# Kernel tuning notes

Hardware: AMD Instinct MI355X
Metric: run time of the kernel (lower is better)

## Reference

```python
import jax, jax.numpy as jnp
import numpy as np

# Model dims (match init_kwargs)
B, S, H = 1, 2048, 1024
E = 16            # n_routed_experts
I = 768           # moe_intermediate_size
TOPK = 4          # num_experts_per_tok
G = 4             # n_group
TOPK_G = 2        # topk_group
SCALE = 2.5       # routed_scaling_factor
N_SHARED = 1      # n_shared_experts


def setup_inputs() -> dict:
    key = jax.random.key(0)
    ks = jax.random.split(key, 9)
    def rn(k, shape, scale=0.02):
        return jax.random.normal(k, shape, dtype=jnp.float32) * scale
    return dict(
        hidden_states=jax.random.normal(ks[0], (B, S, H), dtype=jnp.float32),
        gate_w=rn(ks[1], (E, H)),
        gate_bias=jax.random.normal(ks[2], (E,), dtype=jnp.float32) * 0.1,
        w1=rn(ks[3], (E, I, H)),   # gate_proj weights [out,in]
        w2=rn(ks[4], (E, H, I)),   # down_proj weights
        w3=rn(ks[5], (E, I, H)),   # up_proj weights
        ws1=rn(ks[6], (I * N_SHARED, H)),
        ws2=rn(ks[7], (H, I * N_SHARED)),
        ws3=rn(ks[8], (I * N_SHARED, H)),
    )


def _route(x, gate_w, gate_bias):
    """noaux_tc routing: sigmoid scores + bias, group top-k, top_k experts."""
    n = x.shape[0]
    logits = jnp.einsum('nh,eh->ne', x.astype(jnp.float32), gate_w)  # [N,E]
    scores = jax.nn.sigmoid(logits)
    sb = scores + gate_bias                                          # biased scores
    # group score = sum of top-2 biased scores in each group
    gs = sb.reshape(n, G, E // G)
    group_scores = jnp.sum(jax.lax.top_k(gs, 2)[0], axis=-1)         # [N,G]
    _, gidx = jax.lax.top_k(group_scores, TOPK_G)                    # [N,TOPK_G]
    gmask = jnp.sum(jax.nn.one_hot(gidx, G, dtype=sb.dtype), axis=1) # [N,G]
    emask = jnp.repeat(gmask, E // G, axis=-1)                       # [N,E]
    masked = jnp.where(emask > 0, sb, -jnp.inf)
    _, tidx = jax.lax.top_k(masked, TOPK)                            # [N,TOPK]
    w = jnp.take_along_axis(scores, tidx, axis=1)                    # unbiased weights
    w = w / (jnp.sum(w, axis=-1, keepdims=True) + 1e-20)             # norm_topk_prob
    return tidx, w * SCALE


def reference(hidden_states, gate_w, gate_bias, w1, w2, w3, ws1, ws2, ws3):
    b, s, h = hidden_states.shape
    x = hidden_states.reshape(-1, h)                                 # [N,H]
    tidx, tw = _route(x, gate_w, gate_bias)
    n = x.shape[0]
    # dense combine weights [N,E] (zero for unselected experts)
    combine = jnp.zeros((n, E), x.dtype).at[jnp.arange(n)[:, None], tidx].add(tw)
    # grouped SwiGLU experts (dense-over-experts reference form)
    g = jnp.einsum('nh,eih->nei', x, w1)
    u = jnp.einsum('nh,eih->nei', x, w3)
    hact = jax.nn.silu(g) * u * combine[:, :, None]
    y = jnp.einsum('nei,ehi->nh', hact, w2)
    # shared expert SwiGLU
    shared = jnp.einsum('ni,hi->nh', jax.nn.silu(x @ ws1.T) * (x @ ws3.T), ws2)
    return (y + shared).reshape(b, s, h)
```

## Files before the change

### kernel.cpp

```cpp
#include <hip/hip_runtime.h>
#include <hip/hip_bf16.h>
#include <math.h>

#define N_TOK 2048
#define H_DIM 1024
#define N_EXP 16
#define I_DIM 768
#define TOPK 4
#define SCALE 2.5f
#define MAX_TILES 96

typedef __attribute__((ext_vector_type(8))) short bf16x8;
typedef __attribute__((ext_vector_type(4))) float f32x4;

#define OFF_COUNTS   0
#define OFF_OFFSETS  128
#define OFF_TILES    256
#define OFF_TOKIDS   768
#define OFF_TOKW     (OFF_TOKIDS + N_EXP*N_TOK*4)
#define OFF_XB       (OFF_TOKW + N_EXP*N_TOK*4)
#define OFF_HACT     (OFF_XB + (size_t)N_TOK*H_DIM*2)
#define OFF_GWT      (OFF_HACT + (size_t)N_TOK*(TOPK+1)*I_DIM*2)

__device__ __forceinline__ ushort f2bf(float f) {
    union { __hip_bfloat16 h; ushort u; } cv;
    cv.h = __float2bfloat16(f);
    return cv.u;
}
__device__ __forceinline__ unsigned pack2(float lo, float hi) {
    return (unsigned)f2bf(lo) | ((unsigned)f2bf(hi) << 16);
}
__device__ __forceinline__ void async_copy16(const void* g, void* l) {
    __builtin_amdgcn_global_load_lds(
        (const __attribute__((address_space(1))) unsigned int*)g,
        (__attribute__((address_space(3))) unsigned int*)l, 16, 0, 0);
}

__global__ void k_xconv(const float* __restrict__ x, ushort* __restrict__ xb) {
    int i = blockIdx.x * 256 + threadIdx.x;
    float4 v = ((const float4*)x)[i];
    uint2 p;
    p.x = pack2(v.x, v.y);
    p.y = pack2(v.z, v.w);
    ((uint2*)xb)[i] = p;
}

__global__ void k_gwt(const float* __restrict__ gw, float* __restrict__ gwT) {
    int i = blockIdx.x * 256 + threadIdx.x;
    int k = i >> 4, e = i & 15;
    gwT[i] = gw[e * H_DIM + k];
}

__launch_bounds__(256)
__global__ void k_route(const float* __restrict__ x, const float* __restrict__ gwT,
                        const float* __restrict__ gb,
                        int* __restrict__ counts, int* __restrict__ tok_ids,
                        float* __restrict__ tok_w) {
    __shared__ float lgs[4][N_EXP + 1];
    int tid = threadIdx.x;
    int wv = tid >> 6, lane = tid & 63;
    int e = lane & 15, ks = lane >> 4;
    int n = blockIdx.x * 4 + wv;

    const float* xr = x + (size_t)n * H_DIM + ks * 256;
    const float* wr = gwT + ks * 256 * N_EXP + e;
    float a0 = 0.f, a1 = 0.f, a2 = 0.f, a3 = 0.f;
#pragma unroll 8
    for (int k = 0; k < 256; k += 4) {
        float4 xv = *(const float4*)(xr + k);
        a0 += xv.x * wr[(k + 0) * N_EXP];
        a1 += xv.y * wr[(k + 1) * N_EXP];
        a2 += xv.z * wr[(k + 2) * N_EXP];
        a3 += xv.w * wr[(k + 3) * N_EXP];
    }
    float acc = (a0 + a1) + (a2 + a3);
    acc += __shfl_xor(acc, 16);
    acc += __shfl_xor(acc, 32);
    if (lane < 16) lgs[wv][lane] = acc;
    __syncthreads();

    if (tid < 4) {
        int n2 = blockIdx.x * 4 + tid;
        float sc[N_EXP], sb[N_EXP];
        for (int ee = 0; ee < N_EXP; ee++) {
            float l = lgs[tid][ee];
            sc[ee] = 1.f / (1.f + expf(-l));
            sb[ee] = sc[ee] + gb[ee];
        }
        float gsc[4];
        for (int g = 0; g < 4; g++) {
            float m1 = -1e30f, m2 = -1e30f;
            for (int j = 0; j < 4; j++) {
                float v = sb[4 * g + j];
                if (v > m1) { m2 = m1; m1 = v; }
                else if (v > m2) m2 = v;
            }
            gsc[g] = m1 + m2;
        }
        int g1 = 0;
        for (int g = 1; g < 4; g++) if (gsc[g] > gsc[g1]) g1 = g;
        int g2 = -1;
        for (int g = 0; g < 4; g++) {
            if (g == g1) continue;
            if (g2 < 0 || gsc[g] > gsc[g2]) g2 = g;
        }
        bool allowed[N_EXP];
        for (int ee = 0; ee < N_EXP; ee++) {
            int grp = ee >> 2;
            allowed[ee] = (grp == g1) || (grp == g2);
        }
        int chosen[TOPK];
        float wsum = 0.f;
        for (int k = 0; k < TOPK; k++) {
            int best = -1;
            for (int ee = 0; ee < N_EXP; ee++) {
                if (!allowed[ee]) continue;
                if (best < 0 || sb[ee] > sb[best]) best = ee;
            }
            chosen[k] = best;
            allowed[best] = false;
            wsum += sc[best];
        }
        float inv = SCALE / (wsum + 1e-20f);
        for (int k = 0; k < TOPK; k++) {
            int ee = chosen[k];
            int p = atomicAdd(&counts[ee], 1);
            tok_ids[ee * N_TOK + p] = n2;
            tok_w[ee * N_TOK + p] = sc[ee] * inv;
        }
    }
}

__global__ void k_scan(const int* __restrict__ counts, int* __restrict__ offsets,
                       int* __restrict__ tiles) {
    if (threadIdx.x == 0 && blockIdx.x == 0) {
        int off = 0;
        for (int e = 0; e < N_EXP; e++) { offsets[e] = off; off += counts[e]; }
        offsets[N_EXP] = off;
        int t = 0;
        for (int e = 0; e < N_EXP; e++)
            for (int m0 = 0; m0 < counts[e]; m0 += 128)
                tiles[t++] = e | ((m0 >> 7) << 5);
        for (int m0 = 0; m0 < N_TOK; m0 += 128)
            tiles[t++] = N_EXP | ((m0 >> 7) << 5);
        for (; t < MAX_TILES; t++) tiles[t] = -1;
    }
}

__launch_bounds__(256, 3)
__global__ void k_gateup(const ushort* __restrict__ xb, const float* __restrict__ w1,
                         const float* __restrict__ w3, const float* __restrict__ ws1,
                         const float* __restrict__ ws3, const int* __restrict__ counts,
                         const int* __restrict__ offsets, const int* __restrict__ tiles,
                         const int* __restrict__ tok_ids, const float* __restrict__ tok_w,
                         ushort* __restrict__ hact) {
    int desc = tiles[blockIdx.x];
    if (desc < 0) return;
    int e = desc & 31;
    int m0 = (desc >> 5) * 128;
    int i0 = blockIdx.y * 64;
    int Me = (e == N_EXP) ? N_TOK : counts[e];
    const float* W1 = (e == N_EXP) ? ws1 : w1 + (size_t)e * I_DIM * H_DIM;
    const float* W3 = (e == N_EXP) ? ws3 : w3 + (size_t)e * I_DIM * H_DIM;
    int base = offsets[e];

    __shared__ ushort As[128][64];
    __shared__ ushort Bs[128][64];
    __shared__ float tws[128];

    int tid = threadIdx.x;
    int wv = tid >> 6, lane = tid & 63;
    int seg = lane & 7, rsub = lane >> 3;
    int gch = (seg ^ rsub) * 8;

    if (tid < 128) {
        int r = m0 + tid;
        tws[tid] = (e == N_EXP) ? 1.f : ((r < Me) ? tok_w[e * N_TOK + r] : 0.f);
    }

    const ushort* aptr[4];
#pragma unroll
    for (int j = 0; j < 4; j++) {
        int gr = m0 + wv * 32 + j * 8 + rsub;
        int tok = (e == N_EXP) ? gr : ((gr < Me) ? tok_ids[e * N_TOK + gr] : 0);
        aptr[j] = xb + (size_t)tok * H_DIM + gch;
    }
    const float* bptrf[4];
#pragma unroll
    for (int j = 0; j < 4; j++) {
        int r = wv * 32 + j * 8 + rsub;
        const float* W = (r < 64) ? (W1 + (size_t)(i0 + r) * H_DIM)
                                  : (W3 + (size_t)(i0 + r - 64) * H_DIM);
        bptrf[j] = W + gch;
    }

    int quad = lane >> 4, lr = lane & 15, rx = lr & 7;
    f32x4 acc[2][8] = {};

    const int NK = H_DIM / 64;
    float4 bv0[4], bv1[4];
#pragma unroll
    for (int j = 0; j < 4; j++) {
        bv0[j] = *(const float4*)(bptrf[j]);
        bv1[j] = *(const float4*)(bptrf[j] + 4);
    }
    for (int k = 0; k < NK; k++) {
        int off = k * 64;
#pragma unroll
        for (int j = 0; j < 4; j++) async_copy16(aptr[j] + off, &As[wv * 32 + j * 8][0]);
#pragma unroll
        for (int j = 0; j < 4; j++) {
            uint4 p;
            p.x = pack2(bv0[j].x, bv0[j].y);
            p.y = pack2(bv0[j].z, bv0[j].w);
            p.z = pack2(bv1[j].x, bv1[j].y);
            p.w = pack2(bv1[j].z, bv1[j].w);
            *(uint4*)&Bs[wv * 32 + j * 8 + rsub][seg * 8] = p;
        }
        if (k + 1 < NK) {
#pragma unroll
            for (int j = 0; j < 4; j++) {
                bv0[j] = *(const float4*)(bptrf[j] + off + 64);
                bv1[j] = *(const float4*)(bptrf[j] + off + 68);
            }
        }
        __syncthreads();
#pragma unroll
        for (int ks = 0; ks < 2; ks++) {
            int co = ((ks * 4 + quad) ^ rx) * 8;
            bf16x8 a0 = *(const bf16x8*)&As[wv * 32 + lr][co];
            bf16x8 a1 = *(const bf16x8*)&As[wv * 32 + 16 + lr][co];
#pragma unroll
            for (int ni = 0; ni < 8; ni++) {
                bf16x8 bf = *(const bf16x8*)&Bs[ni * 16 + lr][co];
                acc[0][ni] = __builtin_amdgcn_mfma_f32_16x16x32_bf16(a0, bf, acc[0][ni], 0, 0, 0);
                acc[1][ni] = __builtin_amdgcn_mfma_f32_16x16x32_bf16(a1, bf, acc[1][ni], 0, 0, 0);
            }
        }
        __syncthreads();
    }

#pragma unroll
    for (int mi = 0; mi < 2; mi++) {
#pragma unroll
        for (int ni = 0; ni < 4; ni++) {
            f32x4 g = acc[mi][ni];
            f32x4 u = acc[mi][ni + 4];
#pragma unroll
            for (int rg = 0; rg < 4; rg++) {
                int ml = wv * 32 + mi * 16 + quad * 4 + rg;
                int row = m0 + ml;
                if (row < Me) {
                    float gg = g[rg], uu = u[rg];
                    float act = (gg / (1.f + expf(-gg))) * uu * tws[ml];
                    hact[(size_t)(base + row) * I_DIM + i0 + ni * 16 + lr] = f2bf(act);
                }
            }
        }
    }
}

__launch_bounds__(256, 3)
__global__ void k_down(const ushort* __restrict__ hact, const float* __restrict__ w2,
                       const float* __restrict__ ws2, const int* __restrict__ counts,
                       const int* __restrict__ offsets, const int* __restrict__ tiles,
                       const int* __restrict__ tok_ids, float* __restrict__ out) {
    int desc = tiles[blockIdx.x];
    if (desc < 0) return;
    int e = desc & 31;
    int m0 = (desc >> 5) * 128;
    int h0 = blockIdx.y * 128;
    int Me = (e == N_EXP) ? N_TOK : counts[e];
    const float* W2 = (e == N_EXP) ? ws2 : w2 + (size_t)e * H_DIM * I_DIM;
    int base = offsets[e];

    __shared__ ushort As[128][64];
    __shared__ ushort Bs[128][64];
    __shared__ int toks[128];

    int tid = threadIdx.x;
    int wv = tid >> 6, lane = tid & 63;
    int seg = lane & 7, rsub = lane >> 3;
    int gch = (seg ^ rsub) * 8;

    if (tid < 128) {
        int r = m0 + tid;
        toks[tid] = (e == N_EXP) ? r : ((r < Me) ? tok_ids[e * N_TOK + r] : 0);
    }

    const ushort* aptr[4];
#pragma unroll
    for (int j = 0; j < 4; j++) {
        int row = wv * 32 + j * 8 + rsub;
        aptr[j] = hact + (size_t)(base + m0 + row) * I_DIM + gch;
    }
    const float* bptrf[4];
#pragma unroll
    for (int j = 0; j < 4; j++) {
        int r = wv * 32 + j * 8 + rsub;
        bptrf[j] = W2 + (size_t)(h0 + r) * I_DIM + gch;
    }

    int quad = lane >> 4, lr = lane & 15, rx = lr & 7;
    f32x4 acc[2][8] = {};

    const int NK = I_DIM / 64;
    float4 bv0[4], bv1[4];
#pragma unroll
    for (int j = 0; j < 4; j++) {
        bv0[j] = *(const float4*)(bptrf[j]);
        bv1[j] = *(const float4*)(bptrf[j] + 4);
    }
    for (int k = 0; k < NK; k++) {
        int off = k * 64;
#pragma unroll
        for (int j = 0; j < 4; j++) async_copy16(aptr[j] + off, &As[wv * 32 + j * 8][0]);
#pragma unroll
        for (int j = 0; j < 4; j++) {
            uint4 p;
            p.x = pack2(bv0[j].x, bv0[j].y);
            p.y = pack2(bv0[j].z, bv0[j].w);
            p.z = pack2(bv1[j].x, bv1[j].y);
            p.w = pack2(bv1[j].z, bv1[j].w);
            *(uint4*)&Bs[wv * 32 + j * 8 + rsub][seg * 8] = p;
        }
        if (k + 1 < NK) {
#pragma unroll
            for (int j = 0; j < 4; j++) {
                bv0[j] = *(const float4*)(bptrf[j] + off + 64);
                bv1[j] = *(const float4*)(bptrf[j] + off + 68);
            }
        }
        __syncthreads();
#pragma unroll
        for (int ks = 0; ks < 2; ks++) {
            int co = ((ks * 4 + quad) ^ rx) * 8;
            bf16x8 a0 = *(const bf16x8*)&As[wv * 32 + lr][co];
            bf16x8 a1 = *(const bf16x8*)&As[wv * 32 + 16 + lr][co];
#pragma unroll
            for (int ni = 0; ni < 8; ni++) {
                bf16x8 bf = *(const bf16x8*)&Bs[ni * 16 + lr][co];
                acc[0][ni] = __builtin_amdgcn_mfma_f32_16x16x32_bf16(a0, bf, acc[0][ni], 0, 0, 0);
                acc[1][ni] = __builtin_amdgcn_mfma_f32_16x16x32_bf16(a1, bf, acc[1][ni], 0, 0, 0);
            }
        }
        __syncthreads();
    }

#pragma unroll
    for (int mi = 0; mi < 2; mi++) {
#pragma unroll
        for (int ni = 0; ni < 8; ni++) {
#pragma unroll
            for (int rg = 0; rg < 4; rg++) {
                int ml = wv * 32 + mi * 16 + quad * 4 + rg;
                int row = m0 + ml;
                if (row < Me) {
                    int tok = toks[ml];
                    atomicAdd(&out[(size_t)tok * H_DIM + h0 + ni * 16 + lr],
                              acc[mi][ni][rg]);
                }
            }
        }
    }
}

extern "C" void kernel_launch(void* const* d_in, const int* in_sizes, int n_in,
                              void* d_out, int out_size, void* d_ws, size_t ws_size,
                              hipStream_t stream) {
    const float* x   = (const float*)d_in[0];
    const float* gw  = (const float*)d_in[1];
    const float* gb  = (const float*)d_in[2];
    const float* w1  = (const float*)d_in[3];
    const float* w2  = (const float*)d_in[4];
    const float* w3  = (const float*)d_in[5];
    const float* ws1 = (const float*)d_in[6];
    const float* ws2 = (const float*)d_in[7];
    const float* ws3 = (const float*)d_in[8];
    float* out = (float*)d_out;

    char* wsb = (char*)d_ws;
    int* counts   = (int*)(wsb + OFF_COUNTS);
    int* offsets  = (int*)(wsb + OFF_OFFSETS);
    int* tiles    = (int*)(wsb + OFF_TILES);
    int* tok_ids  = (int*)(wsb + OFF_TOKIDS);
    float* tok_w  = (float*)(wsb + OFF_TOKW);
    ushort* xb    = (ushort*)(wsb + OFF_XB);
    ushort* hact  = (ushort*)(wsb + OFF_HACT);
    float* gwT    = (float*)(wsb + OFF_GWT);

    hipMemsetAsync(wsb, 0, 128, stream);
    hipMemsetAsync(d_out, 0, (size_t)out_size * 4, stream);

    k_xconv<<<N_TOK * H_DIM / 4 / 256, 256, 0, stream>>>(x, xb);
    k_gwt<<<N_EXP * H_DIM / 256, 256, 0, stream>>>(gw, gwT);
    k_route<<<N_TOK / 4, 256, 0, stream>>>(x, gwT, gb, counts, tok_ids, tok_w);
    k_scan<<<1, 1, 0, stream>>>(counts, offsets, tiles);
    {
        dim3 grid(MAX_TILES, I_DIM / 64);
        k_gateup<<<grid, 256, 0, stream>>>(xb, w1, w3, ws1, ws3, counts, offsets,
                                           tiles, tok_ids, tok_w, hact);
    }
    {
        dim3 grid(MAX_TILES, H_DIM / 128);
        k_down<<<grid, 256, 0, stream>>>(hact, w2, ws2, counts, offsets, tiles,
                                         tok_ids, out);
    }
}
```

Before: 364.7 us.

## Batch up to four M-tiles per block in expert GEMMs to reuse weight streams

Each block now handles a job of up to four consecutive 128-row tiles of one expert, looping over them, instead of a single tile. The grids shrink from 96 tile slots to 48 job slots, and the launch bounds rise from 3 to 4 blocks per CU. The intent is to cut per-block setup and raise L2 reuse of the fp32 weight slices, since consecutive tiles of one block read the same weight columns. The cost is fewer blocks in flight (48×12 and 48×8 slots), which risks underfilling the CUs and load imbalance when some experts have many tiles. Weights are still re-read and re-converted to bf16 for every tile.

```diff
diff --git a/kernel.cpp b/kernel.cpp
--- a/kernel.cpp
+++ b/kernel.cpp
@@ -8,14 +8,15 @@
 #define I_DIM 768
 #define TOPK 4
 #define SCALE 2.5f
-#define MAX_TILES 96
+#define MAX_JOBS 48
+#define JOB_MT 4
 
 typedef __attribute__((ext_vector_type(8))) short bf16x8;
 typedef __attribute__((ext_vector_type(4))) float f32x4;
 
 #define OFF_COUNTS   0
 #define OFF_OFFSETS  128
-#define OFF_TILES    256
+#define OFF_JOBS     256
 #define OFF_TOKIDS   768
 #define OFF_TOKW     (OFF_TOKIDS + N_EXP*N_TOK*4)
 #define OFF_XB       (OFF_TOKW + N_EXP*N_TOK*4)
@@ -132,32 +133,37 @@
 }
 
 __global__ void k_scan(const int* __restrict__ counts, int* __restrict__ offsets,
-                       int* __restrict__ tiles) {
+                       int* __restrict__ jobs) {
     if (threadIdx.x == 0 && blockIdx.x == 0) {
         int off = 0;
         for (int e = 0; e < N_EXP; e++) { offsets[e] = off; off += counts[e]; }
         offsets[N_EXP] = off;
         int t = 0;
-        for (int e = 0; e < N_EXP; e++)
-            for (int m0 = 0; m0 < counts[e]; m0 += 128)
-                tiles[t++] = e | ((m0 >> 7) << 5);
-        for (int m0 = 0; m0 < N_TOK; m0 += 128)
-            tiles[t++] = N_EXP | ((m0 >> 7) << 5);
-        for (; t < MAX_TILES; t++) tiles[t] = -1;
-    }
-}
-
-__launch_bounds__(256, 3)
+        for (int e = 0; e < N_EXP; e++) {
+            int nmt = (counts[e] + 127) >> 7;
+            for (int m = 0; m < nmt; m += JOB_MT) {
+                int take = (nmt - m < JOB_MT) ? (nmt - m) : JOB_MT;
+                jobs[t++] = e | (m << 5) | (take << 9);
+            }
+        }
+        for (int m = 0; m < N_TOK / 128; m += JOB_MT)
+            jobs[t++] = N_EXP | (m << 5) | (JOB_MT << 9);
+        for (; t < MAX_JOBS; t++) jobs[t] = -1;
+    }
+}
+
+__launch_bounds__(256, 4)
 __global__ void k_gateup(const ushort* __restrict__ xb, const float* __restrict__ w1,
                          const float* __restrict__ w3, const float* __restrict__ ws1,
                          const float* __restrict__ ws3, const int* __restrict__ counts,
-                         const int* __restrict__ offsets, const int* __restrict__ tiles,
+                         const int* __restrict__ offsets, const int* __restrict__ jobs,
                          const int* __restrict__ tok_ids, const float* __restrict__ tok_w,
                          ushort* __restrict__ hact) {
-    int desc = tiles[blockIdx.x];
+    int desc = jobs[blockIdx.x];
     if (desc < 0) return;
     int e = desc & 31;
-    int m0 = (desc >> 5) * 128;
+    int mt0 = (desc >> 5) & 15;
+    int nmt = desc >> 9;
     int i0 = blockIdx.y * 64;
     int Me = (e == N_EXP) ? N_TOK : counts[e];
     const float* W1 = (e == N_EXP) ? ws1 : w1 + (size_t)e * I_DIM * H_DIM;
@@ -172,19 +178,8 @@
     int wv = tid >> 6, lane = tid & 63;
     int seg = lane & 7, rsub = lane >> 3;
     int gch = (seg ^ rsub) * 8;
-
-    if (tid < 128) {
-        int r = m0 + tid;
-        tws[tid] = (e == N_EXP) ? 1.f : ((r < Me) ? tok_w[e * N_TOK + r] : 0.f);
-    }
-
-    const ushort* aptr[4];
-#pragma unroll
-    for (int j = 0; j < 4; j++) {
-        int gr = m0 + wv * 32 + j * 8 + rsub;
-        int tok = (e == N_EXP) ? gr : ((gr < Me) ? tok_ids[e * N_TOK + gr] : 0);
-        aptr[j] = xb + (size_t)tok * H_DIM + gch;
-    }
+    int quad = lane >> 4, lr = lane & 15, rx = lr & 7;
+
     const float* bptrf[4];
 #pragma unroll
     for (int j = 0; j < 4; j++) {
@@ -194,81 +189,96 @@
         bptrf[j] = W + gch;
     }
 
-    int quad = lane >> 4, lr = lane & 15, rx = lr & 7;
-    f32x4 acc[2][8] = {};
-
-    const int NK = H_DIM / 64;
-    float4 bv0[4], bv1[4];
-#pragma unroll
-    for (int j = 0; j < 4; j++) {
-        bv0[j] = *(const float4*)(bptrf[j]);
-        bv1[j] = *(const float4*)(bptrf[j] + 4);
-    }
-    for (int k = 0; k < NK; k++) {
-        int off = k * 64;
-#pragma unroll
-        for (int j = 0; j < 4; j++) async_copy16(aptr[j] + off, &As[wv * 32 + j * 8][0]);
+    for (int mt = 0; mt < nmt; mt++) {
+        int m0 = (mt0 + mt) * 128;
+        __syncthreads();
+        if (tid < 128) {
+            int r = m0 + tid;
+            tws[tid] = (e == N_EXP) ? 1.f : ((r < Me) ? tok_w[e * N_TOK + r] : 0.f);
+        }
+        const ushort* aptr[4];
 #pragma unroll
         for (int j = 0; j < 4; j++) {
-            uint4 p;
-            p.x = pack2(bv0[j].x, bv0[j].y);
-            p.y = pack2(bv0[j].z, bv0[j].w);
-            p.z = pack2(bv1[j].x, bv1[j].y);
-            p.w = pack2(bv1[j].z, bv1[j].w);
-            *(uint4*)&Bs[wv * 32 + j * 8 + rsub][seg * 8] = p;
-        }
-        if (k + 1 < NK) {
+            int gr = m0 + wv * 32 + j * 8 + rsub;
+            int tok = (e == N_EXP) ? gr : ((gr < Me) ? tok_ids[e * N_TOK + gr] : 0);
+            aptr[j] = xb + (size_t)tok * H_DIM + gch;
+        }
+
+        f32x4 acc[2][8] = {};
+        const int NK = H_DIM / 64;
+        float4 bv0[4], bv1[4];
+#pragma unroll
+        for (int j = 0; j < 4; j++) {
+            bv0[j] = *(const float4*)(bptrf[j]);
+            bv1[j] = *(const float4*)(bptrf[j] + 4);
+        }
+        for (int k = 0; k < NK; k++) {
+            int off = k * 64;
+#pragma unroll
+            for (int j = 0; j < 4; j++) async_copy16(aptr[j] + off, &As[wv * 32 + j * 8][0]);
 #pragma unroll
             for (int j = 0; j < 4; j++) {
-                bv0[j] = *(const float4*)(bptrf[j] + off + 64);
-                bv1[j] = *(const float4*)(bptrf[j] + off + 68);
-            }
-        }
-        __syncthreads();
-#pragma unroll
-        for (int ks = 0; ks < 2; ks++) {
-            int co = ((ks * 4 + quad) ^ rx) * 8;
-            bf16x8 a0 = *(const bf16x8*)&As[wv * 32 + lr][co];
-            bf16x8 a1 = *(const bf16x8*)&As[wv * 32 + 16 + lr][co];
-#pragma unroll
-            for (int ni = 0; ni < 8; ni++) {
-                bf16x8 bf = *(const bf16x8*)&Bs[ni * 16 + lr][co];
-                acc[0][ni] = __builtin_amdgcn_mfma_f32_16x16x32_bf16(a0, bf, acc[0][ni], 0, 0, 0);
-                acc[1][ni] = __builtin_amdgcn_mfma_f32_16x16x32_bf16(a1, bf, acc[1][ni], 0, 0, 0);
-            }
-        }
-        __syncthreads();
-    }
-
-#pragma unroll
-    for (int mi = 0; mi < 2; mi++) {
-#pragma unroll
-        for (int ni = 0; ni < 4; ni++) {
-            f32x4 g = acc[mi][ni];
-            f32x4 u = acc[mi][ni + 4];
-#pragma unroll
-            for (int rg = 0; rg < 4; rg++) {
-                int ml = wv * 32 + mi * 16 + quad * 4 + rg;
-                int row = m0 + ml;
-                if (row < Me) {
-                    float gg = g[rg], uu = u[rg];
-                    float act = (gg / (1.f + expf(-gg))) * uu * tws[ml];
-                    hact[(size_t)(base + row) * I_DIM + i0 + ni * 16 + lr] = f2bf(act);
-                }
-            }
-        }
-    }
-}
-
-__launch_bounds__(256, 3)
+                uint4 p;
+                p.x = pack2(bv0[j].x, bv0[j].y);
+                p.y = pack2(bv0[j].z, bv0[j].w);
+                p.z = pack2(bv1[j].x, bv1[j].y);
+                p.w = pack2(bv1[j].z, bv1[j].w);
+                *(uint4*)&Bs[wv * 32 + j * 8 + rsub][seg * 8] = p;
+            }
+            if (k + 1 < NK) {
+#pragma unroll
+                for (int j = 0; j < 4; j++) {
+                    bv0[j] = *(const float4*)(bptrf[j] + off + 64);
+                    bv1[j] = *(const float4*)(bptrf[j] + off + 68);
+                }
+            }
+            __syncthreads();
+#pragma unroll
+            for (int ks = 0; ks < 2; ks++) {
+                int co = ((ks * 4 + quad) ^ rx) * 8;
+                bf16x8 a0 = *(const bf16x8*)&As[wv * 32 + lr][co];
+                bf16x8 a1 = *(const bf16x8*)&As[wv * 32 + 16 + lr][co];
+#pragma unroll
+                for (int ni = 0; ni < 8; ni++) {
+                    bf16x8 bf = *(const bf16x8*)&Bs[ni * 16 + lr][co];
+                    acc[0][ni] = __builtin_amdgcn_mfma_f32_16x16x32_bf16(a0, bf, acc[0][ni], 0, 0, 0);
+                    acc[1][ni] = __builtin_amdgcn_mfma_f32_16x16x32_bf16(a1, bf, acc[1][ni], 0, 0, 0);
+                }
+            }
+            __syncthreads();
+        }
+
+#pragma unroll
+        for (int mi = 0; mi < 2; mi++) {
+#pragma unroll
+            for (int ni = 0; ni < 4; ni++) {
+                f32x4 g = acc[mi][ni];
+                f32x4 u = acc[mi][ni + 4];
+#pragma unroll
+                for (int rg = 0; rg < 4; rg++) {
+                    int ml = wv * 32 + mi * 16 + quad * 4 + rg;
+                    int row = m0 + ml;
+                    if (row < Me) {
+                        float gg = g[rg], uu = u[rg];
+                        float act = (gg / (1.f + expf(-gg))) * uu * tws[ml];
+                        hact[(size_t)(base + row) * I_DIM + i0 + ni * 16 + lr] = f2bf(act);
+                    }
+                }
+            }
+        }
+    }
+}
+
+__launch_bounds__(256, 4)
 __global__ void k_down(const ushort* __restrict__ hact, const float* __restrict__ w2,
                        const float* __restrict__ ws2, const int* __restrict__ counts,
-                       const int* __restrict__ offsets, const int* __restrict__ tiles,
+                       const int* __restrict__ offsets, const int* __restrict__ jobs,
                        const int* __restrict__ tok_ids, float* __restrict__ out) {
-    int desc = tiles[blockIdx.x];
+    int desc = jobs[blockIdx.x];
     if (desc < 0) return;
     int e = desc & 31;
-    int m0 = (desc >> 5) * 128;
+    int mt0 = (desc >> 5) & 15;
+    int nmt = desc >> 9;
     int h0 = blockIdx.y * 128;
     int Me = (e == N_EXP) ? N_TOK : counts[e];
     const float* W2 = (e == N_EXP) ? ws2 : w2 + (size_t)e * H_DIM * I_DIM;
@@ -282,18 +292,8 @@
     int wv = tid >> 6, lane = tid & 63;
     int seg = lane & 7, rsub = lane >> 3;
     int gch = (seg ^ rsub) * 8;
-
-    if (tid < 128) {
-        int r = m0 + tid;
-        toks[tid] = (e == N_EXP) ? r : ((r < Me) ? tok_ids[e * N_TOK + r] : 0);
-    }
-
-    const ushort* aptr[4];
-#pragma unroll
-    for (int j = 0; j < 4; j++) {
-        int row = wv * 32 + j * 8 + rsub;
-        aptr[j] = hact + (size_t)(base + m0 + row) * I_DIM + gch;
-    }
+    int quad = lane >> 4, lr = lane & 15, rx = lr & 7;
+
     const float* bptrf[4];
 #pragma unroll
     for (int j = 0; j < 4; j++) {
@@ -301,64 +301,77 @@
         bptrf[j] = W2 + (size_t)(h0 + r) * I_DIM + gch;
     }
 
-    int quad = lane >> 4, lr = lane & 15, rx = lr & 7;
-    f32x4 acc[2][8] = {};
-
-    const int NK = I_DIM / 64;
-    float4 bv0[4], bv1[4];
-#pragma unroll
-    for (int j = 0; j < 4; j++) {
-        bv0[j] = *(const float4*)(bptrf[j]);
-        bv1[j] = *(const float4*)(bptrf[j] + 4);
-    }
-    for (int k = 0; k < NK; k++) {
-        int off = k * 64;
-#pragma unroll
-        for (int j = 0; j < 4; j++) async_copy16(aptr[j] + off, &As[wv * 32 + j * 8][0]);
+    for (int mt = 0; mt < nmt; mt++) {
+        int m0 = (mt0 + mt) * 128;
+        __syncthreads();
+        if (tid < 128) {
+            int r = m0 + tid;
+            toks[tid] = (e == N_EXP) ? r : ((r < Me) ? tok_ids[e * N_TOK + r] : 0);
+        }
+        const ushort* aptr[4];
 #pragma unroll
         for (int j = 0; j < 4; j++) {
-            uint4 p;
-            p.x = pack2(bv0[j].x, bv0[j].y);
-            p.y = pack2(bv0[j].z, bv0[j].w);
-            p.z = pack2(bv1[j].x, bv1[j].y);
-            p.w = pack2(bv1[j].z, bv1[j].w);
-            *(uint4*)&Bs[wv * 32 + j * 8 + rsub][seg * 8] = p;
-        }
-        if (k + 1 < NK) {
+            int row = wv * 32 + j * 8 + rsub;
+            aptr[j] = hact + (size_t)(base + m0 + row) * I_DIM + gch;
+        }
+
+        f32x4 acc[2][8] = {};
+        const int NK = I_DIM / 64;
+        float4 bv0[4], bv1[4];
+#pragma unroll
+        for (int j = 0; j < 4; j++) {
+            bv0[j] = *(const float4*)(bptrf[j]);
+            bv1[j] = *(const float4*)(bptrf[j] + 4);
+        }
+        for (int k = 0; k < NK; k++) {
+            int off = k * 64;
+#pragma unroll
+            for (int j = 0; j < 4; j++) async_copy16(aptr[j] + off, &As[wv * 32 + j * 8][0]);
 #pragma unroll
             for (int j = 0; j < 4; j++) {
-                bv0[j] = *(const float4*)(bptrf[j] + off + 64);
-                bv1[j] = *(const float4*)(bptrf[j] + off + 68);
-            }
-        }
-        __syncthreads();
-#pragma unroll
-        for (int ks = 0; ks < 2; ks++) {
-            int co = ((ks * 4 + quad) ^ rx) * 8;
-            bf16x8 a0 = *(const bf16x8*)&As[wv * 32 + lr][co];
-            bf16x8 a1 = *(const bf16x8*)&As[wv * 32 + 16 + lr][co];
+                uint4 p;
+                p.x = pack2(bv0[j].x, bv0[j].y);
+                p.y = pack2(bv0[j].z, bv0[j].w);
+                p.z = pack2(bv1[j].x, bv1[j].y);
+                p.w = pack2(bv1[j].z, bv1[j].w);
+                *(uint4*)&Bs[wv * 32 + j * 8 + rsub][seg * 8] = p;
+            }
+            if (k + 1 < NK) {
+#pragma unroll
+                for (int j = 0; j < 4; j++) {
+                    bv0[j] = *(const float4*)(bptrf[j] + off + 64);
+                    bv1[j] = *(const float4*)(bptrf[j] + off + 68);
+                }
+            }
+            __syncthreads();
+#pragma unroll
+            for (int ks = 0; ks < 2; ks++) {
+                int co = ((ks * 4 + quad) ^ rx) * 8;
+                bf16x8 a0 = *(const bf16x8*)&As[wv * 32 + lr][co];
+                bf16x8 a1 = *(const bf16x8*)&As[wv * 32 + 16 + lr][co];
+#pragma unroll
+                for (int ni = 0; ni < 8; ni++) {
+                    bf16x8 bf = *(const bf16x8*)&Bs[ni * 16 + lr][co];
+                    acc[0][ni] = __builtin_amdgcn_mfma_f32_16x16x32_bf16(a0, bf, acc[0][ni], 0, 0, 0);
+                    acc[1][ni] = __builtin_amdgcn_mfma_f32_16x16x32_bf16(a1, bf, acc[1][ni], 0, 0, 0);
+                }
+            }
+            __syncthreads();
+        }
+
+#pragma unroll
+        for (int mi = 0; mi < 2; mi++) {
 #pragma unroll
             for (int ni = 0; ni < 8; ni++) {
-                bf16x8 bf = *(const bf16x8*)&Bs[ni * 16 + lr][co];
-                acc[0][ni] = __builtin_amdgcn_mfma_f32_16x16x32_bf16(a0, bf, acc[0][ni], 0, 0, 0);
-                acc[1][ni] = __builtin_amdgcn_mfma_f32_16x16x32_bf16(a1, bf, acc[1][ni], 0, 0, 0);
-            }
-        }
-        __syncthreads();
-    }
-
-#pragma unroll
-    for (int mi = 0; mi < 2; mi++) {
-#pragma unroll
-        for (int ni = 0; ni < 8; ni++) {
-#pragma unroll
-            for (int rg = 0; rg < 4; rg++) {
-                int ml = wv * 32 + mi * 16 + quad * 4 + rg;
-                int row = m0 + ml;
-                if (row < Me) {
-                    int tok = toks[ml];
-                    atomicAdd(&out[(size_t)tok * H_DIM + h0 + ni * 16 + lr],
-                              acc[mi][ni][rg]);
+#pragma unroll
+                for (int rg = 0; rg < 4; rg++) {
+                    int ml = wv * 32 + mi * 16 + quad * 4 + rg;
+                    int row = m0 + ml;
+                    if (row < Me) {
+                        int tok = toks[ml];
+                        atomicAdd(&out[(size_t)tok * H_DIM + h0 + ni * 16 + lr],
+                                  acc[mi][ni][rg]);
+                    }
                 }
             }
         }
@@ -382,7 +395,7 @@
     char* wsb = (char*)d_ws;
     int* counts   = (int*)(wsb + OFF_COUNTS);
     int* offsets  = (int*)(wsb + OFF_OFFSETS);
-    int* tiles    = (int*)(wsb + OFF_TILES);
+    int* jobs     = (int*)(wsb + OFF_JOBS);
     int* tok_ids  = (int*)(wsb + OFF_TOKIDS);
     float* tok_w  = (float*)(wsb + OFF_TOKW);
     ushort* xb    = (ushort*)(wsb + OFF_XB);
@@ -395,15 +408,15 @@
     k_xconv<<<N_TOK * H_DIM / 4 / 256, 256, 0, stream>>>(x, xb);
     k_gwt<<<N_EXP * H_DIM / 256, 256, 0, stream>>>(gw, gwT);
     k_route<<<N_TOK / 4, 256, 0, stream>>>(x, gwT, gb, counts, tok_ids, tok_w);
-    k_scan<<<1, 1, 0, stream>>>(counts, offsets, tiles);
+    k_scan<<<1, 1, 0, stream>>>(counts, offsets, jobs);
     {
-        dim3 grid(MAX_TILES, I_DIM / 64);
+        dim3 grid(MAX_JOBS, I_DIM / 64);
         k_gateup<<<grid, 256, 0, stream>>>(xb, w1, w3, ws1, ws3, counts, offsets,
-                                           tiles, tok_ids, tok_w, hact);
+                                           jobs, tok_ids, tok_w, hact);
     }
     {
-        dim3 grid(MAX_TILES, H_DIM / 128);
-        k_down<<<grid, 256, 0, stream>>>(hact, w2, ws2, counts, offsets, tiles,
+        dim3 grid(MAX_JOBS, H_DIM / 128);
+        k_down<<<grid, 256, 0, stream>>>(hact, w2, ws2, counts, offsets, jobs,
                                          tok_ids, out);
     }
 }
```

Result: slower. 605.1 us (+65.9%).

## Schedule expert tiles per XCD with load-balanced grouping for L2 reuse

Applied to the files above, without the earlier changes.

Replaces the 2D tile grid with per-XCD work tables built in the scan kernel: groups of up to four token tiles of the same expert and output slice are assigned to the least-loaded XCD, interleaved so the hardware's round-robin block dispatch lands them there. This aims to improve L2 reuse of expert weight slices and balance work across XCDs, and to remove most empty padded blocks. It makes the single-threaded scan more expensive and relies on the dispatch order mapping block id modulo 8 to an XCD; overflow of a slot table would silently drop tiles.

```diff
diff --git a/kernel.cpp b/kernel.cpp
--- a/kernel.cpp
+++ b/kernel.cpp
@@ -8,15 +8,22 @@
 #define I_DIM 768
 #define TOPK 4
 #define SCALE 2.5f
-#define MAX_TILES 96
+
+#define GU_SLOTS 176
+#define DN_SLOTS 128
+#define GU_TAB (8 * GU_SLOTS)
+#define DN_TAB (8 * DN_SLOTS)
+#define GU_NY (I_DIM / 64)
+#define DN_NY (H_DIM / 128)
 
 typedef __attribute__((ext_vector_type(8))) short bf16x8;
 typedef __attribute__((ext_vector_type(4))) float f32x4;
 
 #define OFF_COUNTS   0
 #define OFF_OFFSETS  128
-#define OFF_TILES    256
-#define OFF_TOKIDS   768
+#define OFF_WGU      256
+#define OFF_WDN      (OFF_WGU + GU_TAB*4)
+#define OFF_TOKIDS   (OFF_WDN + DN_TAB*4)
 #define OFF_TOKW     (OFF_TOKIDS + N_EXP*N_TOK*4)
 #define OFF_XB       (OFF_TOKW + N_EXP*N_TOK*4)
 #define OFF_HACT     (OFF_XB + (size_t)N_TOK*H_DIM*2)
@@ -132,33 +139,62 @@
 }
 
 __global__ void k_scan(const int* __restrict__ counts, int* __restrict__ offsets,
-                       int* __restrict__ tiles) {
-    if (threadIdx.x == 0 && blockIdx.x == 0) {
-        int off = 0;
-        for (int e = 0; e < N_EXP; e++) { offsets[e] = off; off += counts[e]; }
-        offsets[N_EXP] = off;
-        int t = 0;
-        for (int e = 0; e < N_EXP; e++)
-            for (int m0 = 0; m0 < counts[e]; m0 += 128)
-                tiles[t++] = e | ((m0 >> 7) << 5);
-        for (int m0 = 0; m0 < N_TOK; m0 += 128)
-            tiles[t++] = N_EXP | ((m0 >> 7) << 5);
-        for (; t < MAX_TILES; t++) tiles[t] = -1;
-    }
+                       int* __restrict__ wgu, int* __restrict__ wdn) {
+    if (threadIdx.x != 0 || blockIdx.x != 0) return;
+    int off = 0;
+    for (int e = 0; e < N_EXP; e++) { offsets[e] = off; off += counts[e]; }
+    offsets[N_EXP] = off;
+
+    int nx[8];
+    for (int c = 0; c < 8; c++) nx[c] = 0;
+    for (int y = 0; y < GU_NY; y++) {
+        for (int e = 0; e <= N_EXP; e++) {
+            int nmt = (e == N_EXP) ? (N_TOK >> 7) : ((counts[e] + 127) >> 7);
+            for (int m = 0; m < nmt; m += 4) {
+                int take = (nmt - m < 4) ? (nmt - m) : 4;
+                int c = 0;
+                for (int j = 1; j < 8; j++) if (nx[j] < nx[c]) c = j;
+                for (int k = 0; k < take && nx[c] < GU_SLOTS; k++) {
+                    wgu[c + 8 * nx[c]] = e | ((m + k) << 5) | (y << 9);
+                    nx[c]++;
+                }
+            }
+        }
+    }
+    for (int c = 0; c < 8; c++)
+        for (int r = nx[c]; r < GU_SLOTS; r++) wgu[c + 8 * r] = -1;
+
+    for (int c = 0; c < 8; c++) nx[c] = 0;
+    for (int y = 0; y < DN_NY; y++) {
+        for (int e = 0; e <= N_EXP; e++) {
+            int nmt = (e == N_EXP) ? (N_TOK >> 7) : ((counts[e] + 127) >> 7);
+            for (int m = 0; m < nmt; m += 4) {
+                int take = (nmt - m < 4) ? (nmt - m) : 4;
+                int c = 0;
+                for (int j = 1; j < 8; j++) if (nx[j] < nx[c]) c = j;
+                for (int k = 0; k < take && nx[c] < DN_SLOTS; k++) {
+                    wdn[c + 8 * nx[c]] = e | ((m + k) << 5) | (y << 9);
+                    nx[c]++;
+                }
+            }
+        }
+    }
+    for (int c = 0; c < 8; c++)
+        for (int r = nx[c]; r < DN_SLOTS; r++) wdn[c + 8 * r] = -1;
 }
 
 __launch_bounds__(256, 3)
 __global__ void k_gateup(const ushort* __restrict__ xb, const float* __restrict__ w1,
                          const float* __restrict__ w3, const float* __restrict__ ws1,
                          const float* __restrict__ ws3, const int* __restrict__ counts,
-                         const int* __restrict__ offsets, const int* __restrict__ tiles,
+                         const int* __restrict__ offsets, const int* __restrict__ wgu,
                          const int* __restrict__ tok_ids, const float* __restrict__ tok_w,
                          ushort* __restrict__ hact) {
-    int desc = tiles[blockIdx.x];
+    int desc = wgu[blockIdx.x];
     if (desc < 0) return;
     int e = desc & 31;
-    int m0 = (desc >> 5) * 128;
-    int i0 = blockIdx.y * 64;
+    int m0 = ((desc >> 5) & 15) * 128;
+    int i0 = ((desc >> 9) & 15) * 64;
     int Me = (e == N_EXP) ? N_TOK : counts[e];
     const float* W1 = (e == N_EXP) ? ws1 : w1 + (size_t)e * I_DIM * H_DIM;
     const float* W3 = (e == N_EXP) ? ws3 : w3 + (size_t)e * I_DIM * H_DIM;
@@ -263,13 +299,13 @@
 __launch_bounds__(256, 3)
 __global__ void k_down(const ushort* __restrict__ hact, const float* __restrict__ w2,
                        const float* __restrict__ ws2, const int* __restrict__ counts,
-                       const int* __restrict__ offsets, const int* __restrict__ tiles,
+                       const int* __restrict__ offsets, const int* __restrict__ wdn,
                        const int* __restrict__ tok_ids, float* __restrict__ out) {
-    int desc = tiles[blockIdx.x];
+    int desc = wdn[blockIdx.x];
     if (desc < 0) return;
     int e = desc & 31;
-    int m0 = (desc >> 5) * 128;
-    int h0 = blockIdx.y * 128;
+    int m0 = ((desc >> 5) & 15) * 128;
+    int h0 = ((desc >> 9) & 15) * 128;
     int Me = (e == N_EXP) ? N_TOK : counts[e];
     const float* W2 = (e == N_EXP) ? ws2 : w2 + (size_t)e * H_DIM * I_DIM;
     int base = offsets[e];
@@ -382,7 +418,8 @@
     char* wsb = (char*)d_ws;
     int* counts   = (int*)(wsb + OFF_COUNTS);
     int* offsets  = (int*)(wsb + OFF_OFFSETS);
-    int* tiles    = (int*)(wsb + OFF_TILES);
+    int* wgu      = (int*)(wsb + OFF_WGU);
+    int* wdn      = (int*)(wsb + OFF_WDN);
     int* tok_ids  = (int*)(wsb + OFF_TOKIDS);
     float* tok_w  = (float*)(wsb + OFF_TOKW);
     ushort* xb    = (ushort*)(wsb + OFF_XB);
@@ -395,15 +432,9 @@
     k_xconv<<<N_TOK * H_DIM / 4 / 256, 256, 0, stream>>>(x, xb);
     k_gwt<<<N_EXP * H_DIM / 256, 256, 0, stream>>>(gw, gwT);
     k_route<<<N_TOK / 4, 256, 0, stream>>>(x, gwT, gb, counts, tok_ids, tok_w);
-    k_scan<<<1, 1, 0, stream>>>(counts, offsets, tiles);
-    {
-        dim3 grid(MAX_TILES, I_DIM / 64);
-        k_gateup<<<grid, 256, 0, stream>>>(xb, w1, w3, ws1, ws3, counts, offsets,
-                                           tiles, tok_ids, tok_w, hact);
-    }
-    {
-        dim3 grid(MAX_TILES, H_DIM / 128);
-        k_down<<<grid, 256, 0, stream>>>(hact, w2, ws2, counts, offsets, tiles,
-                                         tok_ids, out);
-    }
-}
+    k_scan<<<1, 1, 0, stream>>>(counts, offsets, wgu, wdn);
+    k_gateup<<<GU_TAB, 256, 0, stream>>>(xb, w1, w3, ws1, ws3, counts, offsets,
+                                         wgu, tok_ids, tok_w, hact);
+    k_down<<<DN_TAB, 256, 0, stream>>>(hact, w2, ws2, counts, offsets, wdn,
+                                       tok_ids, out);
+}
```

Measured after the change: 677.7 us. 85.8% more time.
